# Kernel tuning notes

Measured on AMD Instinct MI355X. Metric: run time of the kernel, lower is better.

The kernel has to match this reference:

```python
import jax, jax.numpy as jnp
import numpy as np

EPS = 1e-5

def setup_inputs() -> dict:
    key = jax.random.key(0)
    ks = jax.random.split(key, 12)
    B, L, d_model, d_pair = 2, 384, 1024, 128
    h = jax.random.normal(ks[0], (B, L, d_model), dtype=jnp.float32)
    # torch.nn.Linear params: W [out,in], b [out]
    Wi = jax.random.normal(ks[1], (d_pair, d_model), dtype=jnp.float32) * 0.02
    bi = jnp.zeros((d_pair,), dtype=jnp.float32)
    Wj = jax.random.normal(ks[2], (d_pair, d_model), dtype=jnp.float32) * 0.02
    bj = jnp.zeros((d_pair,), dtype=jnp.float32)
    bilinear_weight = jax.random.normal(ks[3], (d_pair, d_pair, d_pair), dtype=jnp.float32) * 0.02
    gamma = jnp.ones((d_pair,), dtype=jnp.float32)
    beta = jnp.zeros((d_pair,), dtype=jnp.float32)
    mix_w = jax.random.normal(ks[4], (d_pair, d_pair, 3, 3), dtype=jnp.float32) * 0.02  # OIHW
    out_w = jax.random.normal(ks[5], (d_pair, d_pair, 1, 1), dtype=jnp.float32) * 0.05
    out_b = jnp.zeros((d_pair,), dtype=jnp.float32)
    return {"h": h, "Wi": Wi, "bi": bi, "Wj": Wj, "bj": bj,
            "bilinear_weight": bilinear_weight, "gamma": gamma, "beta": beta,
            "mix_w": mix_w, "out_w": out_w, "out_b": out_b}

def _instance_norm(x, gamma, beta):
    # x: [B, C, H, W]; normalize per (b, c) over spatial dims
    mean = jnp.mean(x, axis=(2, 3), keepdims=True)
    var = jnp.var(x, axis=(2, 3), keepdims=True)
    xn = (x - mean) * jax.lax.rsqrt(var + EPS)
    return xn * gamma[None, :, None, None] + beta[None, :, None, None]

def _conv(x, w):
    return jax.lax.conv_general_dilated(
        x, w, window_strides=(1, 1), padding='SAME',
        dimension_numbers=('NCHW', 'OIHW', 'NCHW'))

def reference(h, Wi, bi, Wj, bj, bilinear_weight, gamma, beta, mix_w, out_w, out_b):
    ui = h @ Wi.T + bi  # [B, L, d_pair]
    vj = h @ Wj.T + bj  # [B, L, d_pair]
    # pairwise bilinear: [B, d_pair(k), L, L]
    feat = jnp.einsum('bli,ijk,bmj->bklm', ui, bilinear_weight, vj)
    feat = _instance_norm(feat, gamma, beta)
    feat = jax.nn.relu(feat)
    feat = jax.nn.relu(_conv(feat, mix_w))
    return _conv(feat, out_w) + out_b[None, :, None, None]
```

## Files before the change

### kernel.cpp

```cpp
#include <hip/hip_runtime.h>
#include <hip/hip_bf16.h>
#include <stdint.h>

typedef __bf16 bf16_t;
typedef __bf16 bf16x8 __attribute__((ext_vector_type(8)));
typedef float  f32x4  __attribute__((ext_vector_type(4)));

#define MFMA(a, b, c) __builtin_amdgcn_mfma_f32_16x16x32_bf16((a), (b), (c), 0, 0, 0)

__device__ __forceinline__ void gload_lds16(const void* g, void* l) {
  __builtin_amdgcn_global_load_lds(
      (const __attribute__((address_space(1))) unsigned int*)(g),
      (__attribute__((address_space(3))) unsigned int*)(l), 16, 0, 0);
}

__global__ __launch_bounds__(256) void k_lin2(
    const float* __restrict__ h, const float* __restrict__ Wi,
    const float* __restrict__ bi, const float* __restrict__ Wj,
    const float* __restrict__ bj, bf16_t* __restrict__ ui,
    bf16_t* __restrict__ vj) {
  int m0 = blockIdx.x * 64;
  int which = blockIdx.y;
  const float* W = which ? Wj : Wi;
  const float* bias = which ? bj : bi;
  bf16_t* out = which ? vj : ui;
  __shared__ bf16_t Al[64][136];
  __shared__ bf16_t Bl[128][136];
  int w = threadIdx.x >> 6, ln = threadIdx.x & 63;
  int wr = (w >> 1) * 32, wc = (w & 1) * 64;
  int lr = ln & 15, hi8 = (ln >> 4) * 8, rb = (ln >> 4) * 4;
  f32x4 acc[2][4] = {};
  for (int kc0 = 0; kc0 < 1024; kc0 += 128) {
    __syncthreads();
    for (int c = threadIdx.x; c < 64 * 16; c += 256) {
      int row = c >> 4, col = (c & 15) * 8;
      const float* src = &h[(size_t)(m0 + row) * 1024 + kc0 + col];
      f32x4 a = *(const f32x4*)src, b2 = *(const f32x4*)(src + 4);
      bf16x8 o;
#pragma unroll
      for (int e = 0; e < 4; e++) {
        o[e] = (bf16_t)a[e];
        o[e + 4] = (bf16_t)b2[e];
      }
      *(bf16x8*)&Al[row][col] = o;
    }
    for (int c = threadIdx.x; c < 128 * 16; c += 256) {
      int row = c >> 4, col = (c & 15) * 8;
      const float* src = &W[(size_t)row * 1024 + kc0 + col];
      f32x4 a = *(const f32x4*)src, b2 = *(const f32x4*)(src + 4);
      bf16x8 o;
#pragma unroll
      for (int e = 0; e < 4; e++) {
        o[e] = (bf16_t)a[e];
        o[e + 4] = (bf16_t)b2[e];
      }
      *(bf16x8*)&Bl[row][col] = o;
    }
    __syncthreads();
#pragma unroll
    for (int kc = 0; kc < 128; kc += 32) {
      bf16x8 a0 = *(bf16x8*)&Al[wr + lr][kc + hi8];
      bf16x8 a1 = *(bf16x8*)&Al[wr + 16 + lr][kc + hi8];
#pragma unroll
      for (int fn = 0; fn < 4; fn++) {
        bf16x8 bv = *(bf16x8*)&Bl[wc + fn * 16 + lr][kc + hi8];
        acc[0][fn] = MFMA(a0, bv, acc[0][fn]);
        acc[1][fn] = MFMA(a1, bv, acc[1][fn]);
      }
    }
  }
#pragma unroll
  for (int fm = 0; fm < 2; fm++)
#pragma unroll
    for (int fn = 0; fn < 4; fn++) {
      int col = wc + fn * 16 + lr;
      float bb = bias[col];
#pragma unroll
      for (int r = 0; r < 4; r++) {
        int row = m0 + wr + fm * 16 + rb + r;
        out[row * 128 + col] = (bf16_t)(acc[fm][fn][r] + bb);
      }
    }
}

__global__ __launch_bounds__(256) void k_wt(const float* __restrict__ W,
                                            bf16_t* __restrict__ Wt) {
  int j = blockIdx.x;
  int i0 = blockIdx.y * 32, k0 = blockIdx.z * 32;
  __shared__ float tile[32][33];
  int tx = threadIdx.x & 31, ty = threadIdx.x >> 5;
#pragma unroll
  for (int r = 0; r < 4; r++) {
    int ii = ty + r * 8;
    tile[ii][tx] = W[(size_t)(i0 + ii) * 16384 + j * 128 + (k0 + tx)];
  }
  __syncthreads();
#pragma unroll
  for (int r = 0; r < 4; r++) {
    int kk = ty + r * 8;
    Wt[(size_t)(k0 + kk) * 16384 + j * 128 + (i0 + tx)] = (bf16_t)tile[tx][kk];
  }
}

__global__ __launch_bounds__(256) void k_wc(const float* __restrict__ mw,
                                            bf16_t* __restrict__ Wc2) {
  int idx = blockIdx.x * 256 + threadIdx.x;
  if (idx < 147456) {
    int e = idx & 7, ln = (idx >> 3) & 63, fm = (idx >> 9) & 3;
    int kc = (idx >> 11) & 3, wrh = (idx >> 13) & 1, tap = idx >> 14;
    int oc = wrh * 64 + fm * 16 + (ln & 15);
    int ic = kc * 32 + (ln >> 4) * 8 + e;
    Wc2[idx] = (bf16_t)mw[oc * 1152 + ic * 9 + tap];
  }
}

__global__ __launch_bounds__(256) void k_wo(const float* __restrict__ ow,
                                            bf16_t* __restrict__ Wo2) {
  int idx = blockIdx.x * 256 + threadIdx.x;
  if (idx < 16384) {
    int e = idx & 7, ln = (idx >> 3) & 63, fm = (idx >> 9) & 3;
    int kc = (idx >> 11) & 3, wrh = (idx >> 13) & 1;
    int oc2 = wrh * 64 + fm * 16 + (ln & 15);
    int mc = kc * 32 + (ln >> 4) * 8 + e;
    Wo2[idx] = (bf16_t)ow[oc2 * 128 + mc];
  }
}

__global__ __launch_bounds__(256) void k_tgemm(const bf16_t* __restrict__ A,
                                               const bf16_t* __restrict__ Bt,
                                               bf16_t* __restrict__ T) {
  int m0 = blockIdx.x * 64;
  int n0 = blockIdx.y * 64;
  __shared__ bf16_t Al[64][136], Bl[64][136];
  for (int c = threadIdx.x; c < 64 * 16; c += 256) {
    int row = c >> 4, col = (c & 15) * 8;
    *(uint4*)&Al[row][col] = *(const uint4*)&A[(size_t)(m0 + row) * 128 + col];
    *(uint4*)&Bl[row][col] = *(const uint4*)&Bt[(size_t)(n0 + row) * 128 + col];
  }
  __syncthreads();
  int w = threadIdx.x >> 6, ln = threadIdx.x & 63;
  int wr = (w >> 1) * 32, wc = (w & 1) * 32;
  int lr = ln & 15, hi8 = (ln >> 4) * 8, rb = (ln >> 4) * 4;
  f32x4 acc[2][2] = {};
#pragma unroll
  for (int kc = 0; kc < 128; kc += 32) {
    bf16x8 a0 = *(bf16x8*)&Al[wr + lr][kc + hi8];
    bf16x8 a1 = *(bf16x8*)&Al[wr + 16 + lr][kc + hi8];
    bf16x8 b0 = *(bf16x8*)&Bl[wc + lr][kc + hi8];
    bf16x8 b1 = *(bf16x8*)&Bl[wc + 16 + lr][kc + hi8];
    acc[0][0] = MFMA(a0, b0, acc[0][0]);
    acc[0][1] = MFMA(a0, b1, acc[0][1]);
    acc[1][0] = MFMA(a1, b0, acc[1][0]);
    acc[1][1] = MFMA(a1, b1, acc[1][1]);
  }
#pragma unroll
  for (int fm = 0; fm < 2; fm++)
#pragma unroll
    for (int fn = 0; fn < 2; fn++) {
      int col = n0 + wc + fn * 16 + lr;
#pragma unroll
      for (int r = 0; r < 4; r++) {
        int row = m0 + wr + fm * 16 + rb + r;
        T[(size_t)row * 16384 + col] = (bf16_t)acc[fm][fn][r];
      }
    }
}

__global__ __launch_bounds__(256) void k_feat(const bf16_t* __restrict__ T,
                                              const bf16_t* __restrict__ Vb,
                                              bf16_t* __restrict__ F,
                                              float* __restrict__ part) {
  int bl = blockIdx.x;
  int b = bl / 384;
  __shared__ __align__(16) char sm[52224];
  bf16_t (*Tl)[136] = (bf16_t(*)[136])(sm);
  bf16_t (*Fb)[136] = (bf16_t(*)[136])(sm + 34816);
  float* rs = (float*)(sm);
  float* rq = (float*)(sm + 8192);
  const bf16_t* tsrc = T + (size_t)bl * 16384;
  for (int c = threadIdx.x; c < 128 * 16; c += 256) {
    int row = c >> 4, col = (c & 15) * 8;
    *(uint4*)&Tl[row][col] = *(const uint4*)&tsrc[row * 128 + col];
  }
  __syncthreads();
  int w = threadIdx.x >> 6, ln = threadIdx.x & 63;
  int wr = (w >> 1) * 64, wc = (w & 1) * 32;
  int lr = ln & 15, g = ln >> 4, hi8 = g * 8, rb = g * 4;
  size_t base = (size_t)bl * 384 * 128;
  float s8[8] = {}, q8[8] = {};
  int col8 = threadIdx.x & 15;
  for (int mt = 0; mt < 6; mt++) {
    bf16x8 vf[2][4];
#pragma unroll
    for (int fn = 0; fn < 2; fn++)
#pragma unroll
      for (int kc = 0; kc < 4; kc++) {
        int m = mt * 64 + wc + fn * 16 + lr;
        vf[fn][kc] = *(const bf16x8*)&Vb[(size_t)(b * 384 + m) * 128 +
                                         kc * 32 + hi8];
      }
    f32x4 acc[4][2] = {};
#pragma unroll
    for (int kc = 0; kc < 4; kc++) {
#pragma unroll
      for (int fm = 0; fm < 4; fm++) {
        bf16x8 av = *(bf16x8*)&Tl[wr + fm * 16 + lr][kc * 32 + hi8];
        acc[fm][0] = MFMA(av, vf[0][kc], acc[fm][0]);
        acc[fm][1] = MFMA(av, vf[1][kc], acc[fm][1]);
      }
    }
    __syncthreads();
    union {
      bf16_t h[4];
      uint2 u;
    } pk;
#pragma unroll
    for (int fm = 0; fm < 4; fm++)
#pragma unroll
      for (int fn = 0; fn < 2; fn++) {
        int m = wc + fn * 16 + lr;
        int kb = wr + fm * 16 + rb;
#pragma unroll
        for (int r = 0; r < 4; r++) pk.h[r] = (bf16_t)acc[fm][fn][r];
        *(uint2*)&Fb[m][kb] = pk.u;
      }
    __syncthreads();
    for (int c = threadIdx.x; c < 64 * 16; c += 256) {
      int row = c >> 4;
      uint4 v = *(uint4*)&Fb[row][col8 * 8];
      *(uint4*)&F[base + (size_t)(mt * 64 + row) * 128 + col8 * 8] = v;
      const bf16_t* hp = (const bf16_t*)&v;
#pragma unroll
      for (int e = 0; e < 8; e++) {
        float f = (float)hp[e];
        s8[e] += f;
        q8[e] += f * f;
      }
    }
  }
  int sub = threadIdx.x >> 4;
#pragma unroll
  for (int e = 0; e < 8; e++) {
    rs[(sub * 16 + col8) * 8 + e] = s8[e];
    rq[(sub * 16 + col8) * 8 + e] = q8[e];
  }
  __syncthreads();
  if (threadIdx.x < 128) {
    int k = threadIdx.x, kg = k >> 3, e = k & 7;
    float S = 0.f, Q = 0.f;
#pragma unroll
    for (int s = 0; s < 16; s++) {
      S += rs[(s * 16 + kg) * 8 + e];
      Q += rq[(s * 16 + kg) * 8 + e];
    }
    part[(size_t)bl * 256 + k] = S;
    part[(size_t)bl * 256 + 128 + k] = Q;
  }
}

__global__ __launch_bounds__(64) void k_stats2(const float* __restrict__ part,
                                               const float* __restrict__ gamma,
                                               const float* __restrict__ beta,
                                               float* __restrict__ ss) {
  int k = blockIdx.x, b = blockIdx.y, t = threadIdx.x;
  float S = 0.f, Q = 0.f;
  for (int l = t; l < 384; l += 64) {
    S += part[(size_t)(b * 384 + l) * 256 + k];
    Q += part[(size_t)(b * 384 + l) * 256 + 128 + k];
  }
#pragma unroll
  for (int o = 32; o; o >>= 1) {
    S += __shfl_down(S, o, 64);
    Q += __shfl_down(Q, o, 64);
  }
  if (t == 0) {
    const float inv = 1.0f / 147456.0f;
    float mean = S * inv;
    float var = Q * inv - mean * mean;
    float sc = gamma[k] * rsqrtf(var + 1e-5f);
    ss[b * 256 + k] = sc;
    ss[b * 256 + 128 + k] = beta[k] - mean * sc;
  }
}

__global__ __launch_bounds__(512, 1) void k_conv(
    const bf16_t* __restrict__ Fn, const float* __restrict__ ss,
    const bf16_t* __restrict__ Wc2, const bf16_t* __restrict__ Wo2,
    const float* __restrict__ outb, float* __restrict__ out) {
  int orig = blockIdx.x;
  int wg = (orig & 7) * 96 + (orig >> 3);
  int b = wg / 384;
  int y = wg - b * 384;

  __shared__ __align__(16) char sm[131584];
  char* smB = sm + 32768;

  int tid = threadIdx.x;
  int w = tid >> 6, ln = tid & 63;
  int wrh = w & 1, pxb = (w >> 1) * 96;
  int lr = ln & 15, g = ln >> 4, rb = g * 4;

  int c8 = (tid & 15) * 8;
  float scr[8], shr[8];
  {
    const float* sb = ss + b * 256;
    *(f32x4*)&scr[0] = *(const f32x4*)&sb[c8];
    *(f32x4*)&scr[4] = *(const f32x4*)&sb[c8 + 4];
    *(f32x4*)&shr[0] = *(const f32x4*)&sb[128 + c8];
    *(f32x4*)&shr[4] = *(const f32x4*)&sb[128 + c8 + 4];
  }

  f32x4 acc[4][6] = {};
  for (int dy = 0; dy < 3; dy++) {
    int yy = y + dy - 1;
    bool yok = (yy >= 0 && yy < 384);
    __syncthreads();
    const char* Frow = (const char*)Fn + (size_t)(b * 384 + yy) * 98304;
#pragma unroll
    for (int i = 0; i < 13; i++) {
      int s = tid + i * 512;
      if (s < 6176) {
        int px = s >> 4, c16 = (s & 15) << 4;
        int xx = px - 1;
        bf16x8 o;
        if (yok && xx >= 0 && xx < 384) {
          bf16x8 f = *(const bf16x8*)(Frow + (size_t)xx * 256 + c16);
#pragma unroll
          for (int e = 0; e < 8; e++) {
            float v = (float)f[e] * scr[e] + shr[e];
            o[e] = (bf16_t)(v > 0.f ? v : 0.f);
          }
        } else {
#pragma unroll
          for (int e = 0; e < 8; e++) o[e] = (bf16_t)0.f;
        }
        int byte = (px << 8) + c16;
        *(bf16x8*)(smB + (byte ^ ((px & 7) << 4))) = o;
      }
    }
#pragma unroll
    for (int dx = 0; dx < 3; dx++) {
      if (dx) __syncthreads();
      const char* WcTap = (const char*)Wc2 + (size_t)(dy * 3 + dx) * 32768;
#pragma unroll
      for (int i = 0; i < 4; i++) {
        int o4 = (tid + i * 512) * 16;
        gload_lds16(WcTap + o4, sm + o4);
      }
      __syncthreads();
#pragma unroll
      for (int kc = 0; kc < 4; kc++) {
        bf16x8 av[4], bv[6];
#pragma unroll
        for (int fn = 0; fn < 6; fn++) {
          int row = pxb + fn * 16 + lr + dx;
          int byte = (row << 8) + (kc << 6) + (g << 4);
          bv[fn] = *(const bf16x8*)(smB + (byte ^ ((row & 7) << 4)));
        }
#pragma unroll
        for (int fm = 0; fm < 4; fm++)
          av[fm] = *(const bf16x8*)(sm + wrh * 16384 + kc * 4096 + fm * 1024 +
                                    ln * 16);
#pragma unroll
        for (int fm = 0; fm < 4; fm++)
#pragma unroll
          for (int fn = 0; fn < 6; fn++)
            acc[fm][fn] = MFMA(av[fm], bv[fn], acc[fm][fn]);
      }
    }
  }
  __syncthreads();
#pragma unroll
  for (int i = 0; i < 4; i++) {
    int o4 = (tid + i * 512) * 16;
    gload_lds16((const char*)Wo2 + o4, sm + o4);
  }
  union {
    bf16_t hh[4];
    uint2 u;
  } pk;
#pragma unroll
  for (int fm = 0; fm < 4; fm++)
#pragma unroll
    for (int fn = 0; fn < 6; fn++) {
      int px = pxb + fn * 16 + lr;
      int mcb = wrh * 64 + fm * 16 + rb;
#pragma unroll
      for (int r = 0; r < 4; r++) {
        float v = acc[fm][fn][r];
        pk.hh[r] = (bf16_t)(v > 0.f ? v : 0.f);
      }
      int byte = (px << 8) + (mcb << 1);
      *(uint2*)(smB + (byte ^ ((px & 7) << 4))) = pk.u;
    }
  __syncthreads();
  f32x4 acc2[4][6] = {};
#pragma unroll
  for (int kc = 0; kc < 4; kc++) {
    bf16x8 av[4], bv[6];
#pragma unroll
    for (int fn = 0; fn < 6; fn++) {
      int row = pxb + fn * 16 + lr;
      int byte = (row << 8) + (kc << 6) + (g << 4);
      bv[fn] = *(const bf16x8*)(smB + (byte ^ ((row & 7) << 4)));
    }
#pragma unroll
    for (int fm = 0; fm < 4; fm++)
      av[fm] = *(const bf16x8*)(sm + wrh * 16384 + kc * 4096 + fm * 1024 +
                                ln * 16);
#pragma unroll
    for (int fm = 0; fm < 4; fm++)
#pragma unroll
      for (int fn = 0; fn < 6; fn++)
        acc2[fm][fn] = MFMA(av[fm], bv[fn], acc2[fm][fn]);
  }
  f32x4 obv[4];
#pragma unroll
  for (int fm = 0; fm < 4; fm++)
    obv[fm] = *(const f32x4*)&outb[wrh * 64 + fm * 16 + rb];
#pragma unroll
  for (int fm = 0; fm < 4; fm++)
#pragma unroll
    for (int fn = 0; fn < 6; fn++) {
      int x = pxb + fn * 16 + lr;
#pragma unroll
      for (int r = 0; r < 4; r++) {
        int oc2 = wrh * 64 + fm * 16 + rb + r;
        out[((size_t)(b * 128 + oc2) * 384 + y) * 384 + x] =
            acc2[fm][fn][r] + obv[fm][r];
      }
    }
}

extern "C" void kernel_launch(void* const* d_in, const int* in_sizes, int n_in,
                              void* d_out, int out_size, void* d_ws,
                              size_t ws_size, hipStream_t stream) {
  const float* h = (const float*)d_in[0];
  const float* Wi = (const float*)d_in[1];
  const float* bi = (const float*)d_in[2];
  const float* Wj = (const float*)d_in[3];
  const float* bj = (const float*)d_in[4];
  const float* Wbl = (const float*)d_in[5];
  const float* gamma = (const float*)d_in[6];
  const float* beta = (const float*)d_in[7];
  const float* mw = (const float*)d_in[8];
  const float* ow = (const float*)d_in[9];
  const float* ob = (const float*)d_in[10];
  float* out = (float*)d_out;

  char* ws = (char*)d_ws;
  size_t off = 0;
  auto alloc = [&](size_t bytes) -> void* {
    void* p = ws + off;
    off = (off + bytes + 255) & ~(size_t)255;
    return p;
  };
  bf16_t* ui_b = (bf16_t*)alloc(768 * 128 * 2);
  bf16_t* vj_b = (bf16_t*)alloc(768 * 128 * 2);
  bf16_t* Wt = (bf16_t*)alloc((size_t)2097152 * 2);
  bf16_t* Wc2 = (bf16_t*)alloc((size_t)147456 * 2);
  bf16_t* Wo2 = (bf16_t*)alloc((size_t)16384 * 2);
  bf16_t* T = (bf16_t*)alloc((size_t)768 * 16384 * 2);
  bf16_t* F = (bf16_t*)alloc((size_t)2 * 384 * 384 * 128 * 2);
  float* part = (float*)alloc((size_t)768 * 256 * 4);
  float* ssb = (float*)alloc((size_t)2 * 256 * 4);

  k_lin2<<<dim3(12, 2), 256, 0, stream>>>(h, Wi, bi, Wj, bj, ui_b, vj_b);
  k_wt<<<dim3(128, 4, 4), 256, 0, stream>>>(Wbl, Wt);
  k_wc<<<(147456 + 255) / 256, 256, 0, stream>>>(mw, Wc2);
  k_wo<<<64, 256, 0, stream>>>(ow, Wo2);
  k_tgemm<<<dim3(12, 256), 256, 0, stream>>>(ui_b, Wt, T);
  k_feat<<<768, 256, 0, stream>>>(T, vj_b, F, part);
  k_stats2<<<dim3(128, 2), 64, 0, stream>>>(part, gamma, beta, ssb);
  k_conv<<<768, 512, 0, stream>>>(F, ssb, Wc2, Wo2, ob, out);
}
```

Measured before the change: 219.1 us.

## Load conv weight fragments directly from global into registers, skipping LDS staging

The 3x3 and 1x1 conv weight fragments are now read straight from global memory (L2-resident) into registers per wave, instead of being staged through LDS with global_load_lds. This drops the weight region from shared memory and removes the per-tap __syncthreads barriers, leaving one barrier after the feature row is staged. The cost is more register pressure (a 4x4 array of bf16x8 per tap) and global-load latency that may no longer be hidden before the MFMAs.

```diff
diff --git a/kernel.cpp b/kernel.cpp
--- a/kernel.cpp
+++ b/kernel.cpp
@@ -7,12 +7,6 @@
 typedef float  f32x4  __attribute__((ext_vector_type(4)));
 
 #define MFMA(a, b, c) __builtin_amdgcn_mfma_f32_16x16x32_bf16((a), (b), (c), 0, 0, 0)
-
-__device__ __forceinline__ void gload_lds16(const void* g, void* l) {
-  __builtin_amdgcn_global_load_lds(
-      (const __attribute__((address_space(1))) unsigned int*)(g),
-      (__attribute__((address_space(3))) unsigned int*)(l), 16, 0, 0);
-}
 
 __global__ __launch_bounds__(256) void k_lin2(
     const float* __restrict__ h, const float* __restrict__ Wi,
@@ -292,8 +286,7 @@
   int b = wg / 384;
   int y = wg - b * 384;
 
-  __shared__ __align__(16) char sm[131584];
-  char* smB = sm + 32768;
+  __shared__ __align__(16) char smB[98816];
 
   int tid = threadIdx.x;
   int w = tid >> 6, ln = tid & 63;
@@ -338,19 +331,20 @@
         *(bf16x8*)(smB + (byte ^ ((px & 7) << 4))) = o;
       }
     }
+    __syncthreads();
 #pragma unroll
     for (int dx = 0; dx < 3; dx++) {
-      if (dx) __syncthreads();
-      const char* WcTap = (const char*)Wc2 + (size_t)(dy * 3 + dx) * 32768;
-#pragma unroll
-      for (int i = 0; i < 4; i++) {
-        int o4 = (tid + i * 512) * 16;
-        gload_lds16(WcTap + o4, sm + o4);
-      }
-      __syncthreads();
+      const bf16_t* Atap =
+          Wc2 + (size_t)(dy * 3 + dx) * 16384 + wrh * 8192 + ln * 8;
+      bf16x8 av[4][4];
+#pragma unroll
+      for (int kc = 0; kc < 4; kc++)
+#pragma unroll
+        for (int fm = 0; fm < 4; fm++)
+          av[kc][fm] = *(const bf16x8*)&Atap[kc * 2048 + fm * 512];
 #pragma unroll
       for (int kc = 0; kc < 4; kc++) {
-        bf16x8 av[4], bv[6];
+        bf16x8 bv[6];
 #pragma unroll
         for (int fn = 0; fn < 6; fn++) {
           int row = pxb + fn * 16 + lr + dx;
@@ -359,22 +353,13 @@
         }
 #pragma unroll
         for (int fm = 0; fm < 4; fm++)
-          av[fm] = *(const bf16x8*)(sm + wrh * 16384 + kc * 4096 + fm * 1024 +
-                                    ln * 16);
-#pragma unroll
-        for (int fm = 0; fm < 4; fm++)
 #pragma unroll
           for (int fn = 0; fn < 6; fn++)
-            acc[fm][fn] = MFMA(av[fm], bv[fn], acc[fm][fn]);
-      }
-    }
-  }
-  __syncthreads();
-#pragma unroll
-  for (int i = 0; i < 4; i++) {
-    int o4 = (tid + i * 512) * 16;
-    gload_lds16((const char*)Wo2 + o4, sm + o4);
-  }
+            acc[fm][fn] = MFMA(av[kc][fm], bv[fn], acc[fm][fn]);
+      }
+    }
+  }
+  __syncthreads();
   union {
     bf16_t hh[4];
     uint2 u;
@@ -395,9 +380,14 @@
     }
   __syncthreads();
   f32x4 acc2[4][6] = {};
+  const bf16_t* Awo = Wo2 + wrh * 8192 + ln * 8;
 #pragma unroll
   for (int kc = 0; kc < 4; kc++) {
-    bf16x8 av[4], bv[6];
+    bf16x8 av2[4];
+#pragma unroll
+    for (int fm = 0; fm < 4; fm++)
+      av2[fm] = *(const bf16x8*)&Awo[kc * 2048 + fm * 512];
+    bf16x8 bv[6];
 #pragma unroll
     for (int fn = 0; fn < 6; fn++) {
       int row = pxb + fn * 16 + lr;
@@ -406,13 +396,9 @@
     }
 #pragma unroll
     for (int fm = 0; fm < 4; fm++)
-      av[fm] = *(const bf16x8*)(sm + wrh * 16384 + kc * 4096 + fm * 1024 +
-                                ln * 16);
-#pragma unroll
-    for (int fm = 0; fm < 4; fm++)
 #pragma unroll
       for (int fn = 0; fn < 6; fn++)
-        acc2[fm][fn] = MFMA(av[fm], bv[fn], acc2[fm][fn]);
+        acc2[fm][fn] = MFMA(av2[fm], bv[fn], acc2[fm][fn]);
   }
   f32x4 obv[4];
 #pragma unroll
```

Result: slower. 347.9 us (+58.8%).
